# Optimization experiments

Measured on AMD Instinct MI355X. Metric: run time of the kernel, lower is better.

Reference implementation:

```python
import jax, jax.numpy as jnp
import numpy as np
from jax import lax

B, S, D = 4, 2048, 1024
E = 8           # num_experts
K = 2           # num_experts_per_tok (top-k)
F = 3264        # moe_intermediate_size = ceil(1024*pi/64)*64
NORM_TOPK = True


def setup_inputs() -> dict:
    key = jax.random.key(0)
    ks = jax.random.split(key, 8)
    sd = 0.02
    return {
        "x": jax.random.normal(ks[0], (B, S, D), jnp.float32),
        "gate_w": jax.random.normal(ks[1], (E, D), jnp.float32) * sd,
        "gate_b": jnp.zeros((E,), jnp.float32),
        "up_w": jax.random.normal(ks[2], (E, F, D), jnp.float32) * sd,
        "up_b": jnp.zeros((E, F), jnp.float32),
        "gp_w": jax.random.normal(ks[3], (E, F, D), jnp.float32) * sd,
        "gp_b": jnp.zeros((E, F), jnp.float32),
        "down_w": jax.random.normal(ks[4], (E, D, F), jnp.float32) * sd,
        "down_b": jnp.zeros((E, D), jnp.float32),
    }


def reference(x, gate_w, gate_b, up_w, up_b, gp_w, gp_b, down_w, down_b):
    bs, slen, dim = x.shape
    xf = x.reshape(-1, dim)                      # [N, D]
    N = xf.shape[0]

    # --- router: softmax over experts, top-k gating ---
    scores = jax.nn.softmax(xf @ gate_w.T + gate_b, axis=-1)   # [N, E]
    top_w, top_idx = lax.top_k(scores, K)                       # [N, K]
    if NORM_TOPK:
        top_w = top_w / (top_w.sum(-1, keepdims=True) + 1e-20)

    # per-(token, expert) combine weight: scatter top-k weights into [N, E]
    comb = jnp.zeros((N, E), xf.dtype).at[
        jnp.arange(N)[:, None], top_idx
    ].add(top_w)                                                # [N, E]

    # --- experts: y = sum_e comb[:, e] * FFN_e(x) (scan keeps memory O(N*F)) ---
    def step(acc, p):
        uw, ub, gw, gb, dw, db, w = p
        h = jax.nn.silu((xf @ gw.T + gb) * (xf @ uw.T + ub))    # [N, F]
        return acc + w[:, None] * (h @ dw.T + db), None

    y0 = jnp.zeros_like(xf)
    y, _ = lax.scan(step, y0, (up_w, up_b, gp_w, gp_b, down_w, down_b, comb.T))
    return y.reshape(bs, slen, dim)
```

## Files before the change

kernel.cpp:

```cpp
#include <hip/hip_runtime.h>
#include <cstdint>

#define NTOK 8192
#define DIM  1024
#define NEXP 8
#define NF   3264
#define NPAIR (NTOK*2)
#define TM 128
#define BK 64
#define ASTRIDE (BK+8)
#define MAXTILES 136

typedef __attribute__((ext_vector_type(8))) short short8;
typedef __attribute__((ext_vector_type(4))) float f32x4;

__device__ __forceinline__ unsigned short f2bf(float f){
    unsigned u = __float_as_uint(f);
    return (unsigned short)((u + 0x7FFFu + ((u >> 16) & 1u)) >> 16);
}
__device__ __forceinline__ unsigned pk2(float a, float b){
    return (unsigned)f2bf(a) | ((unsigned)f2bf(b) << 16);
}
__device__ __forceinline__ uint4 cvt8(const float* p){
    const float4* q = (const float4*)p;
    float4 a = q[0], b = q[1];
    uint4 r;
    r.x = pk2(a.x, a.y); r.y = pk2(a.z, a.w);
    r.z = pk2(b.x, b.y); r.w = pk2(b.z, b.w);
    return r;
}

__device__ __forceinline__ void gload16(const void* g, void* l){
    __builtin_amdgcn_global_load_lds(
        (const __attribute__((address_space(1))) unsigned int*)g,
        (__attribute__((address_space(3))) unsigned int*)l,
        16, 0, 0);
}

__global__ __launch_bounds__(256) void k_cvt(const float4* __restrict__ src,
                                             uint2* __restrict__ dst, int n4){
    int i = blockIdx.x * 256 + threadIdx.x;
    if (i >= n4) return;
    float4 a = src[i];
    uint2 r; r.x = pk2(a.x, a.y); r.y = pk2(a.z, a.w);
    dst[i] = r;
}

__global__ __launch_bounds__(256) void k_zero_f4(float4* __restrict__ p, int n4){
    int i = blockIdx.x * 256 + threadIdx.x;
    if (i < n4) p[i] = make_float4(0.f, 0.f, 0.f, 0.f);
}

__global__ void k_zero_ctrl(int* ctrl){
    if (threadIdx.x < 64) ctrl[threadIdx.x] = 0;
}

template<bool XB>
__global__ __launch_bounds__(256) void k_router(const float* __restrict__ x,
        const float* __restrict__ gw, const float* __restrict__ gb,
        int* __restrict__ top_idx, float* __restrict__ top_w, int* __restrict__ ctrl,
        unsigned short* __restrict__ xb){
    int wave = threadIdx.x >> 6;
    int lane = threadIdx.x & 63;
    int n = blockIdx.x * 4 + wave;
    const float* xr = x + (size_t)n * DIM;
    float acc[NEXP];
    #pragma unroll
    for (int e = 0; e < NEXP; e++) acc[e] = 0.f;
    for (int j = lane; j < DIM; j += 64){
        float xv = xr[j];
        if (XB) xb[(size_t)n * DIM + j] = f2bf(xv);
        #pragma unroll
        for (int e = 0; e < NEXP; e++) acc[e] += xv * gw[e * DIM + j];
    }
    #pragma unroll
    for (int e = 0; e < NEXP; e++){
        float v = acc[e];
        #pragma unroll
        for (int off = 32; off > 0; off >>= 1) v += __shfl_xor(v, off);
        acc[e] = v + gb[e];
    }
    if (lane == 0){
        int i0 = 0; float m0 = acc[0];
        #pragma unroll
        for (int e = 1; e < NEXP; e++) if (acc[e] > m0){ m0 = acc[e]; i0 = e; }
        int i1 = -1; float m1 = -3.4e38f;
        #pragma unroll
        for (int e = 0; e < NEXP; e++) if (e != i0 && acc[e] > m1){ m1 = acc[e]; i1 = e; }
        float b  = __expf(m1 - m0);
        float w0 = 1.f / (1.f + b);
        float w1 = b / (1.f + b);
        top_idx[n * 2] = i0; top_idx[n * 2 + 1] = i1;
        top_w[n * 2] = w0;  top_w[n * 2 + 1] = w1;
        atomicAdd(&ctrl[i0], 1);
        atomicAdd(&ctrl[i1], 1);
    }
}

__global__ void k_prefix(int* ctrl){
    int* counts = ctrl; int* offsets = ctrl + 8; int* tileOff = ctrl + 17; int* cursor = ctrl + 26;
    offsets[0] = 0; tileOff[0] = 0;
    for (int e = 0; e < NEXP; e++){
        offsets[e + 1] = offsets[e] + counts[e];
        tileOff[e + 1] = tileOff[e] + (counts[e] + TM - 1) / TM;
        cursor[e] = 0;
    }
}

__global__ __launch_bounds__(256) void k_scatter(const int* __restrict__ top_idx,
        const float* __restrict__ top_w, int* __restrict__ ctrl,
        int* __restrict__ pair_token, float* __restrict__ pair_w){
    const int* offsets = ctrl + 8;
    int* cursor = ctrl + 26;
    int n = blockIdx.x * 256 + threadIdx.x;
    if (n >= NTOK) return;
    #pragma unroll
    for (int k = 0; k < 2; k++){
        int e = top_idx[n * 2 + k];
        int p = atomicAdd(&cursor[e], 1);
        int slot = offsets[e] + p;
        pair_token[slot] = n;
        pair_w[slot] = top_w[n * 2 + k];
    }
}


__global__ __launch_bounds__(256) void k_gemm1_dma(
        const unsigned short* __restrict__ xb,
        const unsigned short* __restrict__ wg, const unsigned short* __restrict__ wu,
        const float* __restrict__ gpb, const float* __restrict__ upb,
        const int* __restrict__ pair_token, const int* __restrict__ ctrl,
        unsigned short* __restrict__ hbuf){
    const int* offsets = ctrl + 8;
    const int* tileOff = ctrl + 17;
    int g = blockIdx.x;
    if (g >= tileOff[NEXP]) return;
    int e = 0;
    while (e < NEXP - 1 && g >= tileOff[e + 1]) e++;
    int row0 = (g - tileOff[e]) * TM;
    int nrows = offsets[e + 1] - offsets[e];
    int base_slot = offsets[e] + row0;
    int f0 = blockIdx.y * 64;
    int lt = blockIdx.x;

    __shared__ __align__(16) unsigned short As[TM][BK];
    __shared__ __align__(16) unsigned short Bs[TM][BK];

    int tid = threadIdx.x;
    int lane = tid & 63;
    int wave = __builtin_amdgcn_readfirstlane(tid >> 6);
    int rsub = lane >> 3;
    int cd = (lane & 7) ^ rsub;

    const unsigned short* a_g[4];
    const unsigned short* b_g[4];
    char* lA[4]; char* lB[4];
    #pragma unroll
    for (int j = 0; j < 4; j++){
        int chunk = wave * 4 + j;
        int row = chunk * 8 + rsub;
        int rr = (row0 + row < nrows) ? row : 0;
        int tok = pair_token[base_slot + rr] & (NTOK - 1);
        a_g[j] = xb + (size_t)tok * DIM + cd * 8;
        int f = f0 + ((row >> 5) << 4) + (row & 15);
        int up = (row >> 4) & 1;
        b_g[j] = (up ? wu : wg) + ((size_t)e * NF + f) * DIM + cd * 8;
        lA[j] = (char*)As + chunk * 1024;
        lB[j] = (char*)Bs + chunk * 1024;
    }

    int wr64 = (wave >> 1) * 64, wc = wave & 1;
    int lr = lane & 15, q = lane >> 4;
    int l7 = lr & 7;

    f32x4 acc[4][4];
    #pragma unroll
    for (int i = 0; i < 4; i++)
        #pragma unroll
        for (int j = 0; j < 4; j++) acc[i][j] = (f32x4){0.f, 0.f, 0.f, 0.f};

    for (int kb = 0; kb < DIM / BK; kb++){
        int k0 = kb * BK;
        #pragma unroll
        for (int j = 0; j < 4; j++) gload16(a_g[j] + k0, lA[j]);
        #pragma unroll
        for (int j = 0; j < 4; j++) gload16(b_g[j] + k0, lB[j]);
        __syncthreads();
        #pragma unroll
        for (int kk = 0; kk < 2; kk++){
            short8 av[4], bv[4];
            #pragma unroll
            for (int mf = 0; mf < 4; mf++){
                int row = wr64 + mf * 16 + lr;
                int c = kk * 4 + q;
                av[mf] = *(const short8*)((const char*)As + row * 128 + ((c ^ l7) * 16));
            }
            #pragma unroll
            for (int nf = 0; nf < 4; nf++){
                int row = wc * 64 + nf * 16 + lr;
                int c = kk * 4 + q;
                bv[nf] = *(const short8*)((const char*)Bs + row * 128 + ((c ^ l7) * 16));
            }
            #pragma unroll
            for (int mf = 0; mf < 4; mf++)
                #pragma unroll
                for (int nf = 0; nf < 4; nf++)
                    acc[mf][nf] = __builtin_amdgcn_mfma_f32_16x16x32_bf16(av[mf], bv[nf], acc[mf][nf], 0, 0, 0);
        }
        __syncthreads();
    }

    #pragma unroll
    for (int mf = 0; mf < 4; mf++){
        #pragma unroll
        for (int fp = 0; fp < 2; fp++){
            int fcol = f0 + (wc * 2 + fp) * 16 + lr;
            float gb_ = gpb[e * NF + fcol];
            float ub_ = upb[e * NF + fcol];
            #pragma unroll
            for (int r = 0; r < 4; r++){
                int m = wr64 + mf * 16 + q * 4 + r;
                if (row0 + m < nrows){
                    float gv = acc[mf][2 * fp][r] + gb_;
                    float uv = acc[mf][2 * fp + 1][r] + ub_;
                    float z = gv * uv;
                    float h = z / (1.f + __expf(-z));
                    hbuf[((size_t)(lt * TM + m)) * NF + fcol] = f2bf(h);
                }
            }
        }
    }
}

__global__ __launch_bounds__(256) void k_gemm2_dma(
        const unsigned short* __restrict__ hbuf,
        const unsigned short* __restrict__ wd, const float* __restrict__ db,
        const int* __restrict__ pair_token, const float* __restrict__ pair_w,
        const int* __restrict__ ctrl, float* __restrict__ out){
    const int* offsets = ctrl + 8;
    const int* tileOff = ctrl + 17;
    int g = blockIdx.x;
    if (g >= tileOff[NEXP]) return;
    int e = 0;
    while (e < NEXP - 1 && g >= tileOff[e + 1]) e++;
    int row0 = (g - tileOff[e]) * TM;
    int nrows = offsets[e + 1] - offsets[e];
    int base_slot = offsets[e] + row0;
    int n0 = blockIdx.y * TM;
    int lt = blockIdx.x;

    __shared__ __align__(16) unsigned short As[TM][BK];
    __shared__ __align__(16) unsigned short Bs[TM][BK];

    int tid = threadIdx.x;
    int lane = tid & 63;
    int wave = __builtin_amdgcn_readfirstlane(tid >> 6);
    int rsub = lane >> 3;
    int cd = (lane & 7) ^ rsub;

    const unsigned short* a_g[4];
    const unsigned short* b_g[4];
    char* lA[4]; char* lB[4];
    #pragma unroll
    for (int j = 0; j < 4; j++){
        int chunk = wave * 4 + j;
        int row = chunk * 8 + rsub;
        a_g[j] = hbuf + ((size_t)(lt * TM + row)) * NF + cd * 8;
        int d = n0 + row;
        b_g[j] = wd + ((size_t)e * DIM + d) * NF + cd * 8;
        lA[j] = (char*)As + chunk * 1024;
        lB[j] = (char*)Bs + chunk * 1024;
    }

    int wr64 = (wave >> 1) * 64, wc = wave & 1, wc64 = (wave & 1) * 64;
    int lr = lane & 15, q = lane >> 4;
    int l7 = lr & 7;

    f32x4 acc[4][4];
    #pragma unroll
    for (int i = 0; i < 4; i++)
        #pragma unroll
        for (int j = 0; j < 4; j++) acc[i][j] = (f32x4){0.f, 0.f, 0.f, 0.f};

    for (int kb = 0; kb < NF / BK; kb++){
        int k0 = kb * BK;
        #pragma unroll
        for (int j = 0; j < 4; j++) gload16(a_g[j] + k0, lA[j]);
        #pragma unroll
        for (int j = 0; j < 4; j++) gload16(b_g[j] + k0, lB[j]);
        __syncthreads();
        #pragma unroll
        for (int kk = 0; kk < 2; kk++){
            short8 av[4], bv[4];
            #pragma unroll
            for (int mf = 0; mf < 4; mf++){
                int row = wr64 + mf * 16 + lr;
                int c = kk * 4 + q;
                av[mf] = *(const short8*)((const char*)As + row * 128 + ((c ^ l7) * 16));
            }
            #pragma unroll
            for (int nf = 0; nf < 4; nf++){
                int row = wc64 + nf * 16 + lr;
                int c = kk * 4 + q;
                bv[nf] = *(const short8*)((const char*)Bs + row * 128 + ((c ^ l7) * 16));
            }
            #pragma unroll
            for (int mf = 0; mf < 4; mf++)
                #pragma unroll
                for (int nf = 0; nf < 4; nf++)
                    acc[mf][nf] = __builtin_amdgcn_mfma_f32_16x16x32_bf16(av[mf], bv[nf], acc[mf][nf], 0, 0, 0);
        }
        __syncthreads();
    }

    #pragma unroll
    for (int mf = 0; mf < 4; mf++){
        #pragma unroll
        for (int r = 0; r < 4; r++){
            int m = wr64 + mf * 16 + q * 4 + r;
            if (row0 + m < nrows){
                int slot = base_slot + m;
                int tok = pair_token[slot] & (NTOK - 1);
                float w = pair_w[slot];
                #pragma unroll
                for (int nf = 0; nf < 4; nf++){
                    int n = n0 + wc * 64 + nf * 16 + lr;
                    float v = w * (acc[mf][nf][r] + db[e * DIM + n]);
                    atomicAdd(&out[(size_t)tok * DIM + n], v);
                }
            }
        }
    }
}

template<bool WB, bool XB>
__global__ __launch_bounds__(256) void k_gemm1(
        const float* __restrict__ xf, const unsigned short* __restrict__ xb,
        const unsigned short* __restrict__ wg, const unsigned short* __restrict__ wu,
        const float* __restrict__ wgf, const float* __restrict__ wuf,
        const float* __restrict__ gpb, const float* __restrict__ upb,
        const int* __restrict__ pair_token, const int* __restrict__ ctrl,
        unsigned short* __restrict__ hbuf, int t0){
    const int* offsets = ctrl + 8;
    const int* tileOff = ctrl + 17;
    int g = t0 + blockIdx.x;
    if (g >= tileOff[NEXP]) return;
    int e = 0;
    while (e < NEXP - 1 && g >= tileOff[e + 1]) e++;
    int row0 = (g - tileOff[e]) * TM;
    int nrows = offsets[e + 1] - offsets[e];
    int base_slot = offsets[e] + row0;
    int f0 = blockIdx.y * 64;
    int lt = blockIdx.x;

    __shared__ unsigned short As[TM][ASTRIDE];
    __shared__ unsigned short Bs[TM][ASTRIDE];

    int tid = threadIdx.x;
    int sr = tid >> 3, sc = tid & 7;

    const unsigned short* a_src[4];
    const float* a_srcf[4];
    bool a_val[4];
    #pragma unroll
    for (int it = 0; it < 4; it++){
        int r = it * 32 + sr;
        bool v = (row0 + r) < nrows;
        int tok = v ? (pair_token[base_slot + r] & (NTOK - 1)) : 0;
        a_val[it] = v;
        if (XB) a_src[it]  = xb + (size_t)tok * DIM + sc * 8;
        else    a_srcf[it] = xf + (size_t)tok * DIM + sc * 8;
    }
    const unsigned short* b_src[4];
    const float* b_srcf[4];
    #pragma unroll
    for (int it = 0; it < 4; it++){
        int br = it * 32 + sr;
        int f = f0 + ((br >> 5) << 4) + (br & 15);
        bool up = (br >> 4) & 1;
        size_t woff = ((size_t)e * NF + f) * DIM + sc * 8;
        if (WB) b_src[it]  = (up ? wu : wg) + woff;
        else    b_srcf[it] = (up ? wuf : wgf) + woff;
    }

    int lane = tid & 63, wave = tid >> 6;
    int wr64 = (wave >> 1) * 64, wc = wave & 1, wc64 = wc * 64;
    int lr = lane & 15, q = lane >> 4;

    f32x4 acc[4][4];
    #pragma unroll
    for (int i = 0; i < 4; i++)
        #pragma unroll
        for (int j = 0; j < 4; j++) acc[i][j] = (f32x4){0.f, 0.f, 0.f, 0.f};

    for (int kb = 0; kb < DIM / BK; kb++){
        int k0 = kb * BK;
        #pragma unroll
        for (int it = 0; it < 4; it++){
            uint4 v = make_uint4(0u, 0u, 0u, 0u);
            if (a_val[it]){
                if (XB) v = *(const uint4*)(a_src[it] + k0);
                else    v = cvt8(a_srcf[it] + k0);
            }
            *(uint4*)&As[it * 32 + sr][sc * 8] = v;
        }
        #pragma unroll
        for (int it = 0; it < 4; it++){
            uint4 v;
            if (WB) v = *(const uint4*)(b_src[it] + k0);
            else    v = cvt8(b_srcf[it] + k0);
            *(uint4*)&Bs[it * 32 + sr][sc * 8] = v;
        }
        __syncthreads();
        #pragma unroll
        for (int kk = 0; kk < 2; kk++){
            short8 av[4], bv[4];
            #pragma unroll
            for (int mf = 0; mf < 4; mf++) av[mf] = *(const short8*)&As[wr64 + mf * 16 + lr][kk * 32 + q * 8];
            #pragma unroll
            for (int nf = 0; nf < 4; nf++) bv[nf] = *(const short8*)&Bs[wc64 + nf * 16 + lr][kk * 32 + q * 8];
            #pragma unroll
            for (int mf = 0; mf < 4; mf++)
                #pragma unroll
                for (int nf = 0; nf < 4; nf++)
                    acc[mf][nf] = __builtin_amdgcn_mfma_f32_16x16x32_bf16(av[mf], bv[nf], acc[mf][nf], 0, 0, 0);
        }
        __syncthreads();
    }

    #pragma unroll
    for (int mf = 0; mf < 4; mf++){
        #pragma unroll
        for (int fp = 0; fp < 2; fp++){
            int fcol = f0 + (wc * 2 + fp) * 16 + lr;
            float gb_ = gpb[e * NF + fcol];
            float ub_ = upb[e * NF + fcol];
            #pragma unroll
            for (int r = 0; r < 4; r++){
                int m = wr64 + mf * 16 + q * 4 + r;
                if (row0 + m < nrows){
                    float gv = acc[mf][2 * fp][r] + gb_;
                    float uv = acc[mf][2 * fp + 1][r] + ub_;
                    float z = gv * uv;
                    float h = z / (1.f + __expf(-z));
                    hbuf[((size_t)(lt * TM + m)) * NF + fcol] = f2bf(h);
                }
            }
        }
    }
}

template<bool WB>
__global__ __launch_bounds__(256) void k_gemm2(
        const unsigned short* __restrict__ hbuf,
        const unsigned short* __restrict__ wd, const float* __restrict__ wdf,
        const float* __restrict__ db,
        const int* __restrict__ pair_token, const float* __restrict__ pair_w,
        const int* __restrict__ ctrl, float* __restrict__ out, int t0){
    const int* offsets = ctrl + 8;
    const int* tileOff = ctrl + 17;
    int g = t0 + blockIdx.x;
    if (g >= tileOff[NEXP]) return;
    int e = 0;
    while (e < NEXP - 1 && g >= tileOff[e + 1]) e++;
    int row0 = (g - tileOff[e]) * TM;
    int nrows = offsets[e + 1] - offsets[e];
    int base_slot = offsets[e] + row0;
    int n0 = blockIdx.y * TM;
    int lt = blockIdx.x;

    __shared__ unsigned short As[TM][ASTRIDE];
    __shared__ unsigned short Bs[TM][ASTRIDE];

    int tid = threadIdx.x;
    int sr = tid >> 3, sc = tid & 7;

    const unsigned short* a_src[4]; bool a_val[4];
    #pragma unroll
    for (int it = 0; it < 4; it++){
        int r = it * 32 + sr;
        a_val[it] = (row0 + r) < nrows;
        a_src[it] = hbuf + ((size_t)(lt * TM + r)) * NF + sc * 8;
    }
    const unsigned short* b_src[4];
    const float* b_srcf[4];
    #pragma unroll
    for (int it = 0; it < 4; it++){
        int d = n0 + it * 32 + sr;
        size_t woff = ((size_t)e * DIM + d) * NF + sc * 8;
        if (WB) b_src[it]  = wd + woff;
        else    b_srcf[it] = wdf + woff;
    }

    int lane = tid & 63, wave = tid >> 6;
    int wr64 = (wave >> 1) * 64, wc = wave & 1, wc64 = wc * 64;
    int lr = lane & 15, q = lane >> 4;

    f32x4 acc[4][4];
    #pragma unroll
    for (int i = 0; i < 4; i++)
        #pragma unroll
        for (int j = 0; j < 4; j++) acc[i][j] = (f32x4){0.f, 0.f, 0.f, 0.f};

    for (int kb = 0; kb < NF / BK; kb++){
        int k0 = kb * BK;
        #pragma unroll
        for (int it = 0; it < 4; it++){
            uint4 v = make_uint4(0u, 0u, 0u, 0u);
            if (a_val[it]) v = *(const uint4*)(a_src[it] + k0);
            *(uint4*)&As[it * 32 + sr][sc * 8] = v;
        }
        #pragma unroll
        for (int it = 0; it < 4; it++){
            uint4 v;
            if (WB) v = *(const uint4*)(b_src[it] + k0);
            else    v = cvt8(b_srcf[it] + k0);
            *(uint4*)&Bs[it * 32 + sr][sc * 8] = v;
        }
        __syncthreads();
        #pragma unroll
        for (int kk = 0; kk < 2; kk++){
            short8 av[4], bv[4];
            #pragma unroll
            for (int mf = 0; mf < 4; mf++) av[mf] = *(const short8*)&As[wr64 + mf * 16 + lr][kk * 32 + q * 8];
            #pragma unroll
            for (int nf = 0; nf < 4; nf++) bv[nf] = *(const short8*)&Bs[wc64 + nf * 16 + lr][kk * 32 + q * 8];
            #pragma unroll
            for (int mf = 0; mf < 4; mf++)
                #pragma unroll
                for (int nf = 0; nf < 4; nf++)
                    acc[mf][nf] = __builtin_amdgcn_mfma_f32_16x16x32_bf16(av[mf], bv[nf], acc[mf][nf], 0, 0, 0);
        }
        __syncthreads();
    }

    #pragma unroll
    for (int mf = 0; mf < 4; mf++){
        #pragma unroll
        for (int r = 0; r < 4; r++){
            int m = wr64 + mf * 16 + q * 4 + r;
            if (row0 + m < nrows){
                int slot = base_slot + m;
                int tok = pair_token[slot] & (NTOK - 1);
                float w = pair_w[slot];
                #pragma unroll
                for (int nf = 0; nf < 4; nf++){
                    int n = n0 + wc64 + nf * 16 + lr;
                    float v = w * (acc[mf][nf][r] + db[e * DIM + n]);
                    atomicAdd(&out[(size_t)tok * DIM + n], v);
                }
            }
        }
    }
}

extern "C" void kernel_launch(void* const* d_in, const int* in_sizes, int n_in,
                              void* d_out, int out_size, void* d_ws, size_t ws_size,
                              hipStream_t stream){
    (void)in_sizes; (void)n_in; (void)out_size;
    const float* x      = (const float*)d_in[0];
    const float* gate_w = (const float*)d_in[1];
    const float* gate_b = (const float*)d_in[2];
    const float* up_w   = (const float*)d_in[3];
    const float* up_b   = (const float*)d_in[4];
    const float* gp_w   = (const float*)d_in[5];
    const float* gp_b   = (const float*)d_in[6];
    const float* down_w = (const float*)d_in[7];
    const float* down_b = (const float*)d_in[8];
    float* out = (float*)d_out;
    char* ws = (char*)d_ws;

    const size_t SZ_XB   = (size_t)NTOK * DIM * 2;
    const size_t SZ_W    = (size_t)NEXP * NF * DIM * 2;
    const size_t TILE_SZ = (size_t)TM * NF * 2;

    size_t off = 0;
    int*   ctrl       = (int*)(ws + off);   off += 256;
    int*   pair_token = (int*)(ws + off);   off += (size_t)NPAIR * 4;
    float* pair_w     = (float*)(ws + off); off += (size_t)NPAIR * 4;
    int*   top_idx    = (int*)(ws + off);   off += (size_t)NTOK * 2 * 4;
    float* top_w      = (float*)(ws + off); off += (size_t)NTOK * 2 * 4;

    size_t rem = (ws_size > off) ? (ws_size - off) : 0;
    bool XB = false, WB = false;
    unsigned short* xb = nullptr;
    unsigned short *wg = nullptr, *wu = nullptr, *wd = nullptr;

    if (rem >= SZ_XB + TILE_SZ){
        XB = true;
        xb = (unsigned short*)(ws + off); off += SZ_XB; rem -= SZ_XB;
    }
    if (rem >= 3 * SZ_W + (size_t)MAXTILES * TILE_SZ){
        WB = true;
        wg = (unsigned short*)(ws + off); off += SZ_W;
        wu = (unsigned short*)(ws + off); off += SZ_W;
        wd = (unsigned short*)(ws + off); off += SZ_W;
        rem -= 3 * SZ_W;
    }
    int TC = (int)((rem / TILE_SZ) < (size_t)MAXTILES ? (rem / TILE_SZ) : (size_t)MAXTILES);
    if (TC < 1) TC = 1;
    unsigned short* hbuf = (unsigned short*)(ws + off);
    int NCH = (MAXTILES + TC - 1) / TC;
    bool FAST = XB && WB && (TC == MAXTILES);

    int out_n4 = NTOK * DIM / 4;
    k_zero_f4<<<(out_n4 + 255) / 256, 256, 0, stream>>>((float4*)out, out_n4);
    k_zero_ctrl<<<1, 64, 0, stream>>>(ctrl);
    if (WB){
        int n4 = NEXP * NF * DIM / 4;
        int gc = (n4 + 255) / 256;
        k_cvt<<<gc, 256, 0, stream>>>((const float4*)gp_w,   (uint2*)wg, n4);
        k_cvt<<<gc, 256, 0, stream>>>((const float4*)up_w,   (uint2*)wu, n4);
        k_cvt<<<gc, 256, 0, stream>>>((const float4*)down_w, (uint2*)wd, n4);
    }
    if (XB) k_router<true ><<<NTOK / 4, 256, 0, stream>>>(x, gate_w, gate_b, top_idx, top_w, ctrl, xb);
    else    k_router<false><<<NTOK / 4, 256, 0, stream>>>(x, gate_w, gate_b, top_idx, top_w, ctrl, xb);
    k_prefix<<<1, 1, 0, stream>>>(ctrl);
    k_scatter<<<NTOK / 256, 256, 0, stream>>>(top_idx, top_w, ctrl, pair_token, pair_w);

    if (FAST){
        dim3 g1(MAXTILES, NF / 64);
        dim3 g2(MAXTILES, DIM / TM);
        k_gemm1_dma<<<g1, 256, 0, stream>>>(xb, wg, wu, gp_b, up_b, pair_token, ctrl, hbuf);
        k_gemm2_dma<<<g2, 256, 0, stream>>>(hbuf, wd, down_b, pair_token, pair_w, ctrl, out);
    } else {
        dim3 g1((unsigned)TC, NF / 64);
        dim3 g2((unsigned)TC, DIM / TM);
        for (int c = 0; c < NCH; c++){
            int t0 = c * TC;
            if (WB){
                if (XB) k_gemm1<true, true ><<<g1, 256, 0, stream>>>(x, xb, wg, wu, nullptr, nullptr, gp_b, up_b, pair_token, ctrl, hbuf, t0);
                else    k_gemm1<true, false><<<g1, 256, 0, stream>>>(x, xb, wg, wu, nullptr, nullptr, gp_b, up_b, pair_token, ctrl, hbuf, t0);
                k_gemm2<true ><<<g2, 256, 0, stream>>>(hbuf, wd, nullptr, down_b, pair_token, pair_w, ctrl, out, t0);
            } else {
                if (XB) k_gemm1<false, true ><<<g1, 256, 0, stream>>>(x, xb, nullptr, nullptr, gp_w, up_w, gp_b, up_b, pair_token, ctrl, hbuf, t0);
                else    k_gemm1<false, false><<<g1, 256, 0, stream>>>(x, xb, nullptr, nullptr, gp_w, up_w, gp_b, up_b, pair_token, ctrl, hbuf, t0);
                k_gemm2<false><<<g2, 256, 0, stream>>>(hbuf, nullptr, down_w, down_b, pair_token, pair_w, ctrl, out, t0);
            }
        }
    }
}
```

Measured before the change: 1.156 ms.

## Replace atomic scatter-add output with per-slot buffer plus combine kernel

The down-projection GEMM now writes weighted per-pair rows into a dense buffer (reusing the gate weight bf16 buffer, which is dead after gemm1) instead of doing float atomicAdd into the output. A new combine kernel sums each token's two rows using an inverse slot map built in scatter, and the output zeroing moves to the fallback path only. Scatter also now aggregates counts per block in shared memory before one global atomic per expert. This removes atomic contention and the zero pass, at the cost of writing and rereading an extra 64MB buffer. Results also become deterministic.

```diff
diff --git a/kernel.cpp b/kernel.cpp
--- a/kernel.cpp
+++ b/kernel.cpp
@@ -109,19 +109,40 @@
 
 __global__ __launch_bounds__(256) void k_scatter(const int* __restrict__ top_idx,
         const float* __restrict__ top_w, int* __restrict__ ctrl,
-        int* __restrict__ pair_token, float* __restrict__ pair_w){
+        int* __restrict__ pair_token, float* __restrict__ pair_w,
+        int* __restrict__ inv_slot){
     const int* offsets = ctrl + 8;
     int* cursor = ctrl + 26;
-    int n = blockIdx.x * 256 + threadIdx.x;
-    if (n >= NTOK) return;
-    #pragma unroll
-    for (int k = 0; k < 2; k++){
-        int e = top_idx[n * 2 + k];
-        int p = atomicAdd(&cursor[e], 1);
-        int slot = offsets[e] + p;
-        pair_token[slot] = n;
-        pair_w[slot] = top_w[n * 2 + k];
-    }
+    __shared__ int lcnt[NEXP];
+    __shared__ int gbase[NEXP];
+    int tid = threadIdx.x;
+    if (tid < NEXP) lcnt[tid] = 0;
+    __syncthreads();
+    int n = blockIdx.x * 256 + tid;
+    int e0 = top_idx[n * 2];
+    int e1 = top_idx[n * 2 + 1];
+    int p0 = atomicAdd(&lcnt[e0], 1);
+    int p1 = atomicAdd(&lcnt[e1], 1);
+    __syncthreads();
+    if (tid < NEXP) gbase[tid] = atomicAdd(&cursor[tid], lcnt[tid]);
+    __syncthreads();
+    int s0 = offsets[e0] + gbase[e0] + p0;
+    int s1 = offsets[e1] + gbase[e1] + p1;
+    pair_token[s0] = n; pair_w[s0] = top_w[n * 2];
+    pair_token[s1] = n; pair_w[s1] = top_w[n * 2 + 1];
+    inv_slot[n * 2] = s0; inv_slot[n * 2 + 1] = s1;
+}
+
+__global__ __launch_bounds__(256) void k_combine(const float* __restrict__ ybuf,
+        const int* __restrict__ inv_slot, float* __restrict__ out){
+    int t = blockIdx.x;
+    int c = threadIdx.x;
+    int s0 = inv_slot[t * 2], s1 = inv_slot[t * 2 + 1];
+    const float4* y0 = (const float4*)(ybuf + (size_t)s0 * DIM);
+    const float4* y1 = (const float4*)(ybuf + (size_t)s1 * DIM);
+    float4 a = y0[c], b = y1[c];
+    float4 r = make_float4(a.x + b.x, a.y + b.y, a.z + b.z, a.w + b.w);
+    ((float4*)(out + (size_t)t * DIM))[c] = r;
 }
 
 
@@ -235,8 +256,8 @@
 __global__ __launch_bounds__(256) void k_gemm2_dma(
         const unsigned short* __restrict__ hbuf,
         const unsigned short* __restrict__ wd, const float* __restrict__ db,
-        const int* __restrict__ pair_token, const float* __restrict__ pair_w,
-        const int* __restrict__ ctrl, float* __restrict__ out){
+        const float* __restrict__ pair_w,
+        const int* __restrict__ ctrl, float* __restrict__ ybuf){
     const int* offsets = ctrl + 8;
     const int* tileOff = ctrl + 17;
     int g = blockIdx.x;
@@ -320,13 +341,12 @@
             int m = wr64 + mf * 16 + q * 4 + r;
             if (row0 + m < nrows){
                 int slot = base_slot + m;
-                int tok = pair_token[slot] & (NTOK - 1);
                 float w = pair_w[slot];
+                float* yr = ybuf + (size_t)slot * DIM;
                 #pragma unroll
                 for (int nf = 0; nf < 4; nf++){
                     int n = n0 + wc * 64 + nf * 16 + lr;
-                    float v = w * (acc[mf][nf][r] + db[e * DIM + n]);
-                    atomicAdd(&out[(size_t)tok * DIM + n], v);
+                    yr[n] = w * (acc[mf][nf][r] + db[e * DIM + n]);
                 }
             }
         }
@@ -580,6 +600,7 @@
     float* pair_w     = (float*)(ws + off); off += (size_t)NPAIR * 4;
     int*   top_idx    = (int*)(ws + off);   off += (size_t)NTOK * 2 * 4;
     float* top_w      = (float*)(ws + off); off += (size_t)NTOK * 2 * 4;
+    int*   inv_slot   = (int*)(ws + off);   off += (size_t)NTOK * 2 * 4;
 
     size_t rem = (ws_size > off) ? (ws_size - off) : 0;
     bool XB = false, WB = false;
@@ -602,9 +623,9 @@
     unsigned short* hbuf = (unsigned short*)(ws + off);
     int NCH = (MAXTILES + TC - 1) / TC;
     bool FAST = XB && WB && (TC == MAXTILES);
+    float* ybuf = (float*)wg;
 
     int out_n4 = NTOK * DIM / 4;
-    k_zero_f4<<<(out_n4 + 255) / 256, 256, 0, stream>>>((float4*)out, out_n4);
     k_zero_ctrl<<<1, 64, 0, stream>>>(ctrl);
     if (WB){
         int n4 = NEXP * NF * DIM / 4;
@@ -616,14 +637,16 @@
     if (XB) k_router<true ><<<NTOK / 4, 256, 0, stream>>>(x, gate_w, gate_b, top_idx, top_w, ctrl, xb);
     else    k_router<false><<<NTOK / 4, 256, 0, stream>>>(x, gate_w, gate_b, top_idx, top_w, ctrl, xb);
     k_prefix<<<1, 1, 0, stream>>>(ctrl);
-    k_scatter<<<NTOK / 256, 256, 0, stream>>>(top_idx, top_w, ctrl, pair_token, pair_w);
+    k_scatter<<<NTOK / 256, 256, 0, stream>>>(top_idx, top_w, ctrl, pair_token, pair_w, inv_slot);
 
     if (FAST){
         dim3 g1(MAXTILES, NF / 64);
         dim3 g2(MAXTILES, DIM / TM);
         k_gemm1_dma<<<g1, 256, 0, stream>>>(xb, wg, wu, gp_b, up_b, pair_token, ctrl, hbuf);
-        k_gemm2_dma<<<g2, 256, 0, stream>>>(hbuf, wd, down_b, pair_token, pair_w, ctrl, out);
+        k_gemm2_dma<<<g2, 256, 0, stream>>>(hbuf, wd, down_b, pair_w, ctrl, ybuf);
+        k_combine<<<NTOK, 256, 0, stream>>>(ybuf, inv_slot, out);
     } else {
+        k_zero_f4<<<(out_n4 + 255) / 256, 256, 0, stream>>>((float4*)out, out_n4);
         dim3 g1((unsigned)TC, NF / 64);
         dim3 g2((unsigned)TC, DIM / TM);
         for (int c = 0; c < NCH; c++){
```

Measured after the change: 1.017 ms. 1.14x faster.
